# Optimization experiments

Hardware: AMD Instinct MI355X
Metric: run time of the kernel (lower is better)

Reference implementation:

```python
import jax, jax.numpy as jnp
import numpy as np

MARGIN = 40.0


def setup_inputs() -> dict:
    key = jax.random.key(0)
    k1, k2 = jax.random.split(key)
    feat = jax.random.normal(k1, (4096, 512), dtype=jnp.float32)
    targets = jax.random.randint(k2, (4096,), 0, 64, dtype=jnp.int64)
    return {"feat": feat, "targets": targets}


def reference(feat, targets):
    # corr: (n, n) Gram matrix of features
    corr = feat @ feat.T
    # mask[i, j] = True if same class
    mask = targets[:, None] == targets[None, :]
    big = jnp.asarray(jnp.finfo(corr.dtype).max, corr.dtype)
    # per-row min over positives, max over negatives
    corr_ap = jnp.min(jnp.where(mask, corr, big), axis=1)
    corr_an = jnp.max(jnp.where(mask, -big, corr), axis=1)
    # MarginRankingLoss(margin=40) with y = 1: mean(relu(-(ap - an) + margin))
    loss = jnp.mean(jax.nn.relu(corr_an - corr_ap + MARGIN))
    return loss
```

## Files before the change

kernel.cpp:

```cpp
#include <hip/hip_runtime.h>
#include <float.h>
#include <stdint.h>


#define N_ROWS 4096
#define D_K    512
#define BT     128
#define BK     64
#define NTB    (N_ROWS / BT)
#define NTILES (NTB * (NTB + 1) / 2)
#define NITER  (D_K / BK)
#define MARGIN 40.0f

typedef __bf16 bf16_t;
typedef bf16_t bf16x8 __attribute__((ext_vector_type(8)));
typedef float  floatx4 __attribute__((ext_vector_type(4)));
typedef unsigned short ushort_t;
typedef ushort_t ushortx8 __attribute__((ext_vector_type(8)));

#define GLOAD_LDS16(g, l)                                        \
    __builtin_amdgcn_global_load_lds(                            \
        (const __attribute__((address_space(1))) void*)(g),      \
        (__attribute__((address_space(3))) void*)(l), 16, 0, 0)

__device__ __forceinline__ ushort_t f2bf_rne(float x) {
    uint32_t u = __builtin_bit_cast(uint32_t, x);
    return (ushort_t)((u + 0x7FFFu + ((u >> 16) & 1u)) >> 16);
}

__device__ __forceinline__ unsigned int f2mono(float x) {
    uint32_t u = __builtin_bit_cast(uint32_t, x);
    return (u & 0x80000000u) ? ~u : (u | 0x80000000u);
}
__device__ __forceinline__ float mono2f(unsigned int m) {
    uint32_t u = (m & 0x80000000u) ? (m ^ 0x80000000u) : ~m;
    return __builtin_bit_cast(float, u);
}

__global__ __launch_bounds__(256) void cast_kernel(
    const float* __restrict__ f, ushort_t* __restrict__ o,
    unsigned int* __restrict__ ap_m, unsigned int* __restrict__ an_m,
    int* __restrict__ counter)
{
    const int gid = blockIdx.x * 256 + threadIdx.x;
    if (gid == 0) *counter = 0;
    if (gid < N_ROWS) { ap_m[gid] = 0xFFFFFFFFu; an_m[gid] = 0u; }

    const int i = gid * 8;
    const float4 v0 = *(const float4*)(f + i);
    const float4 v1 = *(const float4*)(f + i + 4);
    ushortx8 r;
    r[0] = f2bf_rne(v0.x); r[1] = f2bf_rne(v0.y);
    r[2] = f2bf_rne(v0.z); r[3] = f2bf_rne(v0.w);
    r[4] = f2bf_rne(v1.x); r[5] = f2bf_rne(v1.y);
    r[6] = f2bf_rne(v1.z); r[7] = f2bf_rne(v1.w);
    *(ushortx8*)(o + i) = r;
}

__global__ __launch_bounds__(512, 4) void gram_mfma_kernel(
    const ushort_t* __restrict__ fb, const int* __restrict__ tgt,
    unsigned int* __restrict__ ap_m, unsigned int* __restrict__ an_m,
    int* __restrict__ counter, float* __restrict__ out)
{
    __shared__ __align__(16) ushort_t As[2][BT * BK];
    __shared__ __align__(16) ushort_t Bs[2][BT * BK];
    __shared__ int tgI[BT];
    __shared__ int tgJ[BT];
    __shared__ int s_last;

    float* apRed  = (float*)As;
    float* anRed  = apRed  + 4 * BT;
    float* apRedT = anRed  + 4 * BT;
    float* anRedT = apRedT + 2 * BT;

    int bi = 0, rem = blockIdx.x;
    while (rem >= NTB - bi) { rem -= NTB - bi; ++bi; }
    const int bj = bi + rem;

    const int tid  = threadIdx.x;
    const int i0   = bi * BT;
    const int j0   = bj * BT;
    const int lane = tid & 63;
    const int wave = tid >> 6;
    const int wr   = wave >> 2;
    const int wc   = wave & 3;
    const int lr   = lane & 15;
    const int lg   = lane >> 4;
    const int sw   = lr & 7;

    if (tid < BT)            tgI[tid]      = tgt[i0 + tid];
    else if (tid < 2 * BT)   tgJ[tid - BT] = tgt[j0 + tid - BT];

    const int srow = tid >> 3;
    const int schk = (tid & 7) ^ (srow & 7);
    const size_t gA0 = (size_t)(i0 + srow) * D_K + schk * 8;
    const size_t gB0 = (size_t)(j0 + srow) * D_K + schk * 8;
    const size_t gHi = (size_t)64 * D_K;

#define STAGE(buf, kk) do {                                          \
        char* aD = (char*)As[buf]; char* bD = (char*)Bs[buf];        \
        GLOAD_LDS16(fb + gA0 + (kk),       aD + tid * 16);           \
        GLOAD_LDS16(fb + gA0 + gHi + (kk), aD + 8192 + tid * 16);    \
        GLOAD_LDS16(fb + gB0 + (kk),       bD + tid * 16);           \
        GLOAD_LDS16(fb + gB0 + gHi + (kk), bD + 8192 + tid * 16);    \
    } while (0)

    floatx4 acc[4][2];
#pragma unroll
    for (int a = 0; a < 4; ++a)
#pragma unroll
        for (int b = 0; b < 2; ++b) acc[a][b] = (floatx4)0.0f;

    STAGE(0, 0);
    __syncthreads();

    int cur = 0;
#pragma unroll
    for (int t = 0; t < NITER; ++t) {
        if (t + 1 < NITER) STAGE(cur ^ 1, (t + 1) * BK);

        const ushort_t* Acur = As[cur];
        const ushort_t* Bcur = Bs[cur];
#pragma unroll
        for (int h = 0; h < 2; ++h) {
            bf16x8 af[4], bfr[2];
            const int pc = ((h * 4 + lg) ^ sw) * 8;
#pragma unroll
            for (int rg = 0; rg < 4; ++rg)
                af[rg] = *(const bf16x8*)(Acur + (wr * 64 + rg * 16 + lr) * BK + pc);
#pragma unroll
            for (int cg = 0; cg < 2; ++cg)
                bfr[cg] = *(const bf16x8*)(Bcur + (wc * 32 + cg * 16 + lr) * BK + pc);
#pragma unroll
            for (int rg = 0; rg < 4; ++rg)
#pragma unroll
                for (int cg = 0; cg < 2; ++cg)
                    acc[rg][cg] = __builtin_amdgcn_mfma_f32_16x16x32_bf16(
                        af[rg], bfr[cg], acc[rg][cg], 0, 0, 0);
        }
        if (t + 1 < NITER) {
            __syncthreads();
            cur ^= 1;
        }
    }

    int tj[2];
#pragma unroll
    for (int cg = 0; cg < 2; ++cg) tj[cg] = tgJ[wc * 32 + cg * 16 + lr];

    float apT[2], anT[2];
#pragma unroll
    for (int cg = 0; cg < 2; ++cg) { apT[cg] = FLT_MAX; anT[cg] = -FLT_MAX; }

#pragma unroll
    for (int rg = 0; rg < 4; ++rg) {
#pragma unroll
        for (int r = 0; r < 4; ++r) {
            const int rloc = wr * 64 + rg * 16 + lg * 4 + r;
            const int ti = tgI[rloc];
            float vap = FLT_MAX, van = -FLT_MAX;
#pragma unroll
            for (int cg = 0; cg < 2; ++cg) {
                const float v = acc[rg][cg][r];
                if (ti == tj[cg]) { vap = fminf(vap, v); apT[cg] = fminf(apT[cg], v); }
                else              { van = fmaxf(van, v); anT[cg] = fmaxf(anT[cg], v); }
            }
#pragma unroll
            for (int m = 1; m < 16; m <<= 1) {
                vap = fminf(vap, __shfl_xor(vap, m));
                van = fmaxf(van, __shfl_xor(van, m));
            }
            if (lr == 0) { apRed[wc * BT + rloc] = vap; anRed[wc * BT + rloc] = van; }
        }
    }
#pragma unroll
    for (int cg = 0; cg < 2; ++cg) {
        float vap = apT[cg], van = anT[cg];
        vap = fminf(vap, __shfl_xor(vap, 16)); van = fmaxf(van, __shfl_xor(van, 16));
        vap = fminf(vap, __shfl_xor(vap, 32)); van = fmaxf(van, __shfl_xor(van, 32));
        if (lg == 0) {
            apRedT[wr * BT + wc * 32 + cg * 16 + lr] = vap;
            anRedT[wr * BT + wc * 32 + cg * 16 + lr] = van;
        }
    }
    __syncthreads();

    if (tid < BT) {
        const float ap = fminf(fminf(apRed[0 * BT + tid], apRed[1 * BT + tid]),
                               fminf(apRed[2 * BT + tid], apRed[3 * BT + tid]));
        const float an = fmaxf(fmaxf(anRed[0 * BT + tid], anRed[1 * BT + tid]),
                               fmaxf(anRed[2 * BT + tid], anRed[3 * BT + tid]));
        atomicMin(ap_m + i0 + tid, f2mono(ap));
        atomicMax(an_m + i0 + tid, f2mono(an));
        if (bi != bj) {
            atomicMin(ap_m + j0 + tid,
                      f2mono(fminf(apRedT[0 * BT + tid], apRedT[1 * BT + tid])));
            atomicMax(an_m + j0 + tid,
                      f2mono(fmaxf(anRedT[0 * BT + tid], anRedT[1 * BT + tid])));
        }
    }

    __syncthreads();
    if (tid == 0) {
        __threadfence();
        s_last = (atomicAdd(counter, 1) == NTILES - 1) ? 1 : 0;
    }
    __syncthreads();

    if (s_last) {
        __threadfence();
        float local = 0.0f;
#pragma unroll
        for (int q = 0; q < N_ROWS / 512; ++q) {
            const int r = q * 512 + tid;
            const float ap = mono2f(atomicOr(ap_m + r, 0u));
            const float an = mono2f(atomicOr(an_m + r, 0u));
            const float v  = an - ap + MARGIN;
            local += (v > 0.0f) ? v : 0.0f;
        }
#pragma unroll
        for (int m = 32; m >= 1; m >>= 1) local += __shfl_down(local, m);
        float* fin = (float*)Bs;
        if (lane == 0) fin[wave] = local;
        __syncthreads();
        if (tid == 0) {
            float s = 0.0f;
#pragma unroll
            for (int w = 0; w < 8; ++w) s += fin[w];
            out[0] = s * (1.0f / N_ROWS);
        }
    }
#undef STAGE
}

extern "C" void kernel_launch(void* const* d_in, const int* in_sizes, int n_in,
                              void* d_out, int out_size, void* d_ws, size_t ws_size,
                              hipStream_t stream)
{
    const float* feat = (const float*)d_in[0];
    const int*   tgt  = (const int*)d_in[1];

    ushort_t*     fb   = (ushort_t*)d_ws;
    unsigned int* ap_m = (unsigned int*)(fb + (size_t)N_ROWS * D_K);
    unsigned int* an_m = ap_m + N_ROWS;
    int*          counter = (int*)(an_m + N_ROWS);

    cast_kernel<<<(N_ROWS * D_K) / (256 * 8), 256, 0, stream>>>(
        feat, fb, ap_m, an_m, counter);
    gram_mfma_kernel<<<NTILES, 512, 0, stream>>>(
        fb, tgt, ap_m, an_m, counter, (float*)d_out);
}
```

Baseline: 95.54 us.

## Drop LDS double buffering in favour of single buffer and higher occupancy

Replaces the double-buffered LDS staging of A and B tiles with a single buffer, loading each K-slice, syncing, computing, and syncing again. This halves LDS per block (64KB to 32KB) and raises the launch-bounds occupancy hint from 4 to 6, so more blocks can be resident and hide load latency across blocks. In exchange, global-to-LDS loads no longer overlap with MFMA work inside a block, and each iteration now has two barriers.

New measurement: 85.67 us (median of 2 runs). 10.3% less time.

```diff
diff --git a/kernel.cpp b/kernel.cpp
--- a/kernel.cpp
+++ b/kernel.cpp
@@ -9,7 +9,6 @@
 #define BK     64
 #define NTB    (N_ROWS / BT)
 #define NTILES (NTB * (NTB + 1) / 2)
-#define NITER  (D_K / BK)
 #define MARGIN 40.0f
 
 typedef __bf16 bf16_t;
@@ -57,13 +56,13 @@
     *(ushortx8*)(o + i) = r;
 }
 
-__global__ __launch_bounds__(512, 4) void gram_mfma_kernel(
+__global__ __launch_bounds__(512, 6) void gram_mfma_kernel(
     const ushort_t* __restrict__ fb, const int* __restrict__ tgt,
     unsigned int* __restrict__ ap_m, unsigned int* __restrict__ an_m,
     int* __restrict__ counter, float* __restrict__ out)
 {
-    __shared__ __align__(16) ushort_t As[2][BT * BK];
-    __shared__ __align__(16) ushort_t Bs[2][BT * BK];
+    __shared__ __align__(16) ushort_t As[BT * BK];
+    __shared__ __align__(16) ushort_t Bs[BT * BK];
     __shared__ int tgI[BT];
     __shared__ int tgJ[BT];
     __shared__ int s_last;
@@ -96,14 +95,8 @@
     const size_t gA0 = (size_t)(i0 + srow) * D_K + schk * 8;
     const size_t gB0 = (size_t)(j0 + srow) * D_K + schk * 8;
     const size_t gHi = (size_t)64 * D_K;
-
-#define STAGE(buf, kk) do {                                          \
-        char* aD = (char*)As[buf]; char* bD = (char*)Bs[buf];        \
-        GLOAD_LDS16(fb + gA0 + (kk),       aD + tid * 16);           \
-        GLOAD_LDS16(fb + gA0 + gHi + (kk), aD + 8192 + tid * 16);    \
-        GLOAD_LDS16(fb + gB0 + (kk),       bD + tid * 16);           \
-        GLOAD_LDS16(fb + gB0 + gHi + (kk), bD + 8192 + tid * 16);    \
-    } while (0)
+    char* AsB = (char*)As;
+    char* BsB = (char*)Bs;
 
     floatx4 acc[4][2];
 #pragma unroll
@@ -111,26 +104,23 @@
 #pragma unroll
         for (int b = 0; b < 2; ++b) acc[a][b] = (floatx4)0.0f;
 
-    STAGE(0, 0);
-    __syncthreads();
-
-    int cur = 0;
-#pragma unroll
-    for (int t = 0; t < NITER; ++t) {
-        if (t + 1 < NITER) STAGE(cur ^ 1, (t + 1) * BK);
-
-        const ushort_t* Acur = As[cur];
-        const ushort_t* Bcur = Bs[cur];
+    for (int k0 = 0; k0 < D_K; k0 += BK) {
+        GLOAD_LDS16(fb + gA0 + k0,       AsB + tid * 16);
+        GLOAD_LDS16(fb + gA0 + gHi + k0, AsB + 8192 + tid * 16);
+        GLOAD_LDS16(fb + gB0 + k0,       BsB + tid * 16);
+        GLOAD_LDS16(fb + gB0 + gHi + k0, BsB + 8192 + tid * 16);
+        __syncthreads();
+
 #pragma unroll
         for (int h = 0; h < 2; ++h) {
             bf16x8 af[4], bfr[2];
             const int pc = ((h * 4 + lg) ^ sw) * 8;
 #pragma unroll
             for (int rg = 0; rg < 4; ++rg)
-                af[rg] = *(const bf16x8*)(Acur + (wr * 64 + rg * 16 + lr) * BK + pc);
+                af[rg] = *(const bf16x8*)(As + (wr * 64 + rg * 16 + lr) * BK + pc);
 #pragma unroll
             for (int cg = 0; cg < 2; ++cg)
-                bfr[cg] = *(const bf16x8*)(Bcur + (wc * 32 + cg * 16 + lr) * BK + pc);
+                bfr[cg] = *(const bf16x8*)(Bs + (wc * 32 + cg * 16 + lr) * BK + pc);
 #pragma unroll
             for (int rg = 0; rg < 4; ++rg)
 #pragma unroll
@@ -138,10 +128,7 @@
                     acc[rg][cg] = __builtin_amdgcn_mfma_f32_16x16x32_bf16(
                         af[rg], bfr[cg], acc[rg][cg], 0, 0, 0);
         }
-        if (t + 1 < NITER) {
-            __syncthreads();
-            cur ^= 1;
-        }
+        __syncthreads();
     }
 
     int tj[2];
@@ -230,7 +217,6 @@
             out[0] = s * (1.0f / N_ROWS);
         }
     }
-#undef STAGE
 }
 
 extern "C" void kernel_launch(void* const* d_in, const int* in_sizes, int n_in,
```
